# Kernel optimization log

Measured on AMD Instinct MI355X. Metric: run time of the kernel, lower is better.

Reference implementation:

```python
import jax, jax.numpy as jnp
import numpy as np

D_MODEL = 768
N_HEADS = 12
NUM_EXPERTS = 4
TOP_K = 2
SPAN_LEN = 64
GATE_HIDDEN = 128


def setup_inputs() -> dict:
    key = jax.random.key(0)
    ks = jax.random.split(key, 14)
    B, T, C, E = 4, 4096, D_MODEL, NUM_EXPERTS
    s = 0.02
    return {
        "hidden_states": jax.random.normal(ks[0], (B, T, C), jnp.float32),
        "Wq": jax.random.normal(ks[1], (E, C, C), jnp.float32) * s,
        "bq": jnp.zeros((E, C), jnp.float32),
        "Wk": jax.random.normal(ks[2], (E, C, C), jnp.float32) * s,
        "bk": jnp.zeros((E, C), jnp.float32),
        "Wv": jax.random.normal(ks[3], (E, C, C), jnp.float32) * s,
        "bv": jnp.zeros((E, C), jnp.float32),
        "gW1": jax.random.normal(ks[4], (GATE_HIDDEN, C), jnp.float32) * s,
        "gb1": jnp.zeros((GATE_HIDDEN,), jnp.float32),
        "gW2": jax.random.normal(ks[5], (E, GATE_HIDDEN), jnp.float32) * s,
        "gb2": jnp.zeros((E,), jnp.float32),
        "Wo": jax.random.normal(ks[6], (C, C), jnp.float32) * s,
        "bo": jnp.zeros((C,), jnp.float32),
    }


def _moe_proj(w, x, W, b):
    # per-expert projection then gate-weighted sum over experts
    # x: (B,N,S,C), W: (E,O,C), w: (B,N,E)
    proj = jnp.einsum("bnsc,eoc->ebnso", x, W)          # (E,B,N,S,C)
    out = jnp.einsum("bne,ebnso->bnso", w, proj)
    out = out + jnp.einsum("bne,eo->bno", w, b)[:, :, None, :]
    return out


def reference(hidden_states, Wq, bq, Wk, bk, Wv, bv, gW1, gb1, gW2, gb2, Wo, bo):
    B, T, C = hidden_states.shape
    S, H, E, K = SPAN_LEN, N_HEADS, NUM_EXPERTS, TOP_K
    Dh = C // H
    N = T // S  # T is a multiple of span_len -> no padding, all-ones masks
    x = hidden_states.reshape(B, N, S, C)

    # gating: mean-pool per span -> MLP -> top-k softmax scattered to E slots
    pooled = x.mean(axis=2)                                  # (B,N,C)
    h = jax.nn.relu(pooled @ gW1.T + gb1)
    logits = h @ gW2.T + gb2                                 # (B,N,E)
    vals, idx = jax.lax.top_k(logits, K)
    sm = jax.nn.softmax(vals, axis=-1)                       # (B,N,K)
    w = jnp.sum(jax.nn.one_hot(idx, E, dtype=sm.dtype) * sm[..., None], axis=-2)  # (B,N,E)
    entropy = -jnp.mean(jnp.sum(w * jnp.log(jnp.clip(w, 1e-9)), axis=-1))

    # gate-weighted expert QKV projections
    q = _moe_proj(w, x, Wq, bq).reshape(B, N, S, H, Dh)
    k = _moe_proj(w, x, Wk, bk).reshape(B, N, S, H, Dh)
    v = _moe_proj(w, x, Wv, bv).reshape(B, N, S, H, Dh)

    # per-span attention (mask is all ones; dropout in eval mode)
    scores = jnp.einsum("bnshd,bnthd->bnhst", q, k) / jnp.sqrt(jnp.float32(Dh))
    attn = jax.nn.softmax(scores, axis=-1)
    out = jnp.einsum("bnhst,bnthd->bnshd", attn, v).reshape(B, T, C)
    out = out @ Wo.T + bo
    return out, entropy
```

## Files before the change

### kernel.cpp

```cpp
#include <hip/hip_runtime.h>
#include <hip/hip_bf16.h>
#include <hip/hip_fp16.h>

typedef _Float16 f16;
typedef _Float16 f16x8 __attribute__((ext_vector_type(8)));
typedef _Float16 f16x4 __attribute__((ext_vector_type(4)));
typedef float f32x4 __attribute__((ext_vector_type(4)));

constexpr int B = 4;
constexpr int T = 4096;
constexpr int C = 768;
constexpr int NH = 12;
constexpr int DH = 64;
constexpr int E = 4;
constexpr int SPAN = 64;
constexpr int N = T / SPAN;
constexpr int BN = B * N;
constexpr int GH = 128;
constexpr int BTC = B * T * C;

constexpr int U_WE = E * C * C / 8;
constexpr int U_WO = C * C / 8;
constexpr int U_WTOT = 3 * U_WE + U_WO;

#define LGKM_BARRIER()                                      \
    do {                                                    \
        asm volatile("s_waitcnt lgkmcnt(0)" ::: "memory");  \
        __builtin_amdgcn_s_barrier();                       \
        __builtin_amdgcn_sched_barrier(0);                  \
    } while (0)

__global__ __launch_bounds__(768) void cvt_x_pool(
    const float* __restrict__ x, f16* __restrict__ x16,
    float* __restrict__ pooled) {
    int span = blockIdx.x;
    int tid = threadIdx.x;
    int u = tid % 96, rg = tid / 96;
    __shared__ float part[8][C];

    const float* xb = x + (size_t)span * SPAN * C;
    f16x8* xo = (f16x8*)x16 + (size_t)span * 6144;
    int kt = u >> 2, lg = u & 3;
    float a8[8] = {};
    #pragma unroll
    for (int j = 0; j < 8; ++j) {
        int r = rg * 8 + j;
        const float4* s = (const float4*)(xb + (size_t)r * C + u * 8);
        float4 A = s[0], Bv = s[1];
        f16x8 o;
        o[0] = (f16)A.x;  o[1] = (f16)A.y;  o[2] = (f16)A.z;  o[3] = (f16)A.w;
        o[4] = (f16)Bv.x; o[5] = (f16)Bv.y; o[6] = (f16)Bv.z; o[7] = (f16)Bv.w;
        int m = r >> 4, lr = r & 15;
        xo[(kt * 4 + m) * 64 + lg * 16 + lr] = o;
        a8[0] += A.x;  a8[1] += A.y;  a8[2] += A.z;  a8[3] += A.w;
        a8[4] += Bv.x; a8[5] += Bv.y; a8[6] += Bv.z; a8[7] += Bv.w;
    }
    #pragma unroll
    for (int j = 0; j < 8; ++j) part[rg][u * 8 + j] = a8[j];
    __syncthreads();
    float s = 0.f;
    #pragma unroll
    for (int g = 0; g < 8; ++g) s += part[g][tid];
    pooled[(size_t)span * C + tid] = s * (1.f / 64.f);
}

__global__ void cvt_w(const float* __restrict__ Wq, const float* __restrict__ Wk,
                      const float* __restrict__ Wv, const float* __restrict__ Wo,
                      f16* __restrict__ Wq16, f16* __restrict__ Wk16,
                      f16* __restrict__ Wv16, f16* __restrict__ Wo16) {
    int i = blockIdx.x * blockDim.x + threadIdx.x;
    int stride = gridDim.x * blockDim.x;
    for (; i < U_WTOT; i += stride) {
        const float* src; f16* dst; int u;
        bool frag = true;
        if (i < U_WE)               { src = Wq; dst = Wq16; u = i; }
        else if (i < 2 * U_WE)      { src = Wk; dst = Wk16; u = i - U_WE; }
        else if (i < 3 * U_WE)      { src = Wv; dst = Wv16; u = i - 2 * U_WE; }
        else                        { src = Wo; dst = Wo16; u = i - 3 * U_WE; frag = false; }
        float4 a = ((const float4*)src)[2 * u];
        float4 b = ((const float4*)src)[2 * u + 1];
        f16x8 o;
        o[0] = (f16)a.x; o[1] = (f16)a.y; o[2] = (f16)a.z; o[3] = (f16)a.w;
        o[4] = (f16)b.x; o[5] = (f16)b.y; o[6] = (f16)b.z; o[7] = (f16)b.w;
        if (frag) {
            int e   = u / (C * C / 8);
            int rem = u - e * (C * C / 8);
            int orow = rem / 96;
            int ku   = rem - orow * 96;
            int cb = orow >> 6, nn = (orow >> 4) & 3, lr = orow & 15;
            int kt = ku >> 2, lg = ku & 3;
            ((f16x8*)dst)[(size_t)(e * 12 + cb) * 6144 + (kt * 4 + nn) * 64 + lg * 16 + lr] = o;
        } else {
            ((f16x8*)dst)[u] = o;
        }
    }
}

__global__ __launch_bounds__(128) void gate_mlp(
    const float* __restrict__ pooled,
    const float* __restrict__ gW1, const float* __restrict__ gb1,
    const float* __restrict__ gW2, const float* __restrict__ gb2,
    int* __restrict__ eidx, float* __restrict__ ewts,
    float* __restrict__ ent_partial) {
    int span = blockIdx.x;
    int tid = threadIdx.x;
    __shared__ float pl[C];
    __shared__ float h[GH];
    __shared__ float logits[E];

    for (int c = tid; c < C; c += 128) pl[c] = pooled[(size_t)span * C + c];
    __syncthreads();

    {
        float acc = gb1[tid];
        const float* wrow = gW1 + (size_t)tid * C;
        #pragma unroll 8
        for (int c = 0; c < C; ++c) acc += pl[c] * wrow[c];
        h[tid] = acc > 0.f ? acc : 0.f;
    }
    __syncthreads();

    if (tid < E) {
        float acc = gb2[tid];
        const float* wrow = gW2 + (size_t)tid * GH;
        #pragma unroll 8
        for (int j = 0; j < GH; ++j) acc += h[j] * wrow[j];
        logits[tid] = acc;
    }
    __syncthreads();

    if (tid == 0) {
        int i0 = 0; float v0 = logits[0];
        for (int e = 1; e < E; ++e) { if (logits[e] > v0) { v0 = logits[e]; i0 = e; } }
        int i1 = -1; float v1 = -3.0e38f;
        for (int e = 0; e < E; ++e) { if (e != i0 && logits[e] > v1) { v1 = logits[e]; i1 = e; } }
        float bq_ = expf(v1 - v0);
        float s = 1.f + bq_;
        float sm0 = 1.f / s;
        float sm1 = bq_ / s;
        eidx[span * 2 + 0] = i0;
        eidx[span * 2 + 1] = i1;
        ewts[span * 2 + 0] = sm0;
        ewts[span * 2 + 1] = sm1;
        float p0 = fmaxf(sm0, 1e-9f), p1 = fmaxf(sm1, 1e-9f);
        ent_partial[span] = sm0 * logf(p0) + sm1 * logf(p1);
    }
}

__global__ void entropy_kernel(const float* __restrict__ ent_partial, float* __restrict__ out_ent) {
    __shared__ float sh[256];
    int tid = threadIdx.x;
    sh[tid] = ent_partial[tid];
    __syncthreads();
    for (int s = 128; s > 0; s >>= 1) {
        if (tid < s) sh[tid] += sh[tid + s];
        __syncthreads();
    }
    if (tid == 0) *out_ent = -sh[0] * (1.0f / (float)BN);
}

__global__ __launch_bounds__(256, 3) void qkv_mfma(
    const f16* __restrict__ xh,
    const f16* __restrict__ Wq16, const float* __restrict__ bq,
    const f16* __restrict__ Wk16, const float* __restrict__ bk,
    const f16* __restrict__ Wv16, const float* __restrict__ bv,
    const int* __restrict__ eidx, const float* __restrict__ ewts,
    f16* __restrict__ q16, f16* __restrict__ k16, f16* __restrict__ vt)
{
    int span  = blockIdx.x;
    int otile = blockIdx.y;
    int proj  = blockIdx.z;

    const f16* W; const float* bias; f16* out;
    if (proj == 0)      { W = Wq16; bias = bq; out = q16; }
    else if (proj == 1) { W = Wk16; bias = bk; out = k16; }
    else                { W = Wv16; bias = bv; out = vt; }

    int e0 = eidx[span * 2 + 0], e1 = eidx[span * 2 + 1];
    float w0 = ewts[span * 2 + 0], w1 = ewts[span * 2 + 1];
    f16 w0h = (f16)w0, w1h = (f16)w1;

    int tid = threadIdx.x;
    int lane = tid & 63, wv = tid >> 6;
    int lr = lane & 15, lg = lane >> 4;
    int cb = otile * 4 + wv;

    const f16x8* xu  = (const f16x8*)xh + (size_t)span * 6144 + lane;
    const f16x8* wu0 = (const f16x8*)W + ((size_t)e0 * 12 + cb) * 6144 + lane;
    const f16x8* wu1 = (const f16x8*)W + ((size_t)e1 * 12 + cb) * 6144 + lane;

    f32x4 acc[4][4] = {};

    #pragma unroll 4
    for (int kt = 0; kt < 24; ++kt) {
        f16x8 af[4], bf[4];
        #pragma unroll
        for (int m = 0; m < 4; ++m) af[m] = xu[(kt * 4 + m) * 64];
        #pragma unroll
        for (int n = 0; n < 4; ++n) {
            f16x8 b0 = wu0[(kt * 4 + n) * 64];
            f16x8 b1 = wu1[(kt * 4 + n) * 64];
            bf[n] = b0 * w0h + b1 * w1h;
        }
        #pragma unroll
        for (int m = 0; m < 4; ++m)
            #pragma unroll
            for (int n = 0; n < 4; ++n)
                acc[m][n] = __builtin_amdgcn_mfma_f32_16x16x32_f16(af[m], bf[n], acc[m][n], 0, 0, 0);
    }

    if (proj == 2) {
        f16* vtb = out + (size_t)span * C * 64;
        #pragma unroll
        for (int n = 0; n < 4; ++n) {
            int col = cb * 64 + n * 16 + lr;
            float be = w0 * bias[(size_t)e0 * C + col] + w1 * bias[(size_t)e1 * C + col];
            #pragma unroll
            for (int m = 0; m < 4; ++m) {
                f16x4 pk;
                #pragma unroll
                for (int r = 0; r < 4; ++r) pk[r] = (f16)(acc[m][n][r] + be);
                *(f16x4*)&vtb[(size_t)col * 64 + m * 16 + lg * 4] = pk;
            }
        }
    } else {
        f16* outb = out + (size_t)span * 64 * C;
        #pragma unroll
        for (int n = 0; n < 4; ++n) {
            int col = cb * 64 + n * 16 + lr;
            float be = w0 * bias[(size_t)e0 * C + col] + w1 * bias[(size_t)e1 * C + col];
            #pragma unroll
            for (int m = 0; m < 4; ++m) {
                #pragma unroll
                for (int r = 0; r < 4; ++r) {
                    int row = m * 16 + lg * 4 + r;
                    outb[(size_t)row * C + col] = (f16)(acc[m][n][r] + be);
                }
            }
        }
    }
}

__global__ __launch_bounds__(256) void attn_mfma(
    const f16* __restrict__ q16, const f16* __restrict__ k16,
    const f16* __restrict__ vt, f16* __restrict__ a16)
{
    int h = blockIdx.x, span = blockIdx.y;
    __shared__ __align__(16) f16 Klds[64 * 72];
    __shared__ __align__(16) f16 Vlds[64 * 72];
    __shared__ __align__(16) f16 Plds[64 * 72];

    int tid = threadIdx.x;
    int lane = tid & 63, mt = tid >> 6;
    int lr = lane & 15, lg = lane >> 4;

    const f16x8* ku = (const f16x8*)k16;
    const f16x8* vu = (const f16x8*)vt;
    #pragma unroll
    for (int i = 0; i < 2; ++i) {
        int id = tid + i * 256;
        int r = id >> 3, u = id & 7;
        *(f16x8*)&Klds[r * 72 + u * 8] = ku[(size_t)span * 6144 + (size_t)r * 96 + h * 8 + u];
        *(f16x8*)&Vlds[r * 72 + u * 8] = vu[(size_t)span * 6144 + (size_t)(h * 64 + r) * 8 + u];
    }
    const f16x8* qu = (const f16x8*)q16;
    f16x8 qa[2];
    #pragma unroll
    for (int kk = 0; kk < 2; ++kk)
        qa[kk] = qu[(size_t)span * 6144 + (size_t)(mt * 16 + lr) * 96 + h * 8 + kk * 4 + lg];

    LGKM_BARRIER();

    f32x4 accs[4] = {};
    #pragma unroll
    for (int nt = 0; nt < 4; ++nt) {
        #pragma unroll
        for (int kk = 0; kk < 2; ++kk) {
            f16x8 kb = *(const f16x8*)&Klds[(nt * 16 + lr) * 72 + kk * 32 + lg * 8];
            accs[nt] = __builtin_amdgcn_mfma_f32_16x16x32_f16(qa[kk], kb, accs[nt], 0, 0, 0);
        }
    }

    #pragma unroll
    for (int nt = 0; nt < 4; ++nt) accs[nt] *= 0.125f;
    f32x4 m4;
    #pragma unroll
    for (int r = 0; r < 4; ++r)
        m4[r] = fmaxf(fmaxf(accs[0][r], accs[1][r]), fmaxf(accs[2][r], accs[3][r]));
    #pragma unroll
    for (int st = 1; st < 16; st <<= 1) {
        #pragma unroll
        for (int r = 0; r < 4; ++r) m4[r] = fmaxf(m4[r], __shfl_xor(m4[r], st));
    }
    f32x4 ps[4];
    f32x4 sum4 = {0.f, 0.f, 0.f, 0.f};
    #pragma unroll
    for (int nt = 0; nt < 4; ++nt)
        #pragma unroll
        for (int r = 0; r < 4; ++r) {
            ps[nt][r] = __expf(accs[nt][r] - m4[r]);
            sum4[r] += ps[nt][r];
        }
    #pragma unroll
    for (int st = 1; st < 16; st <<= 1) {
        #pragma unroll
        for (int r = 0; r < 4; ++r) sum4[r] += __shfl_xor(sum4[r], st);
    }
    f32x4 inv4;
    #pragma unroll
    for (int r = 0; r < 4; ++r) inv4[r] = 1.0f / sum4[r];

    #pragma unroll
    for (int nt = 0; nt < 4; ++nt)
        #pragma unroll
        for (int r = 0; r < 4; ++r)
            Plds[(mt * 16 + lg * 4 + r) * 72 + nt * 16 + lr] = (f16)ps[nt][r];

    LGKM_BARRIER();

    f16x8 pa[2];
    #pragma unroll
    for (int kkt = 0; kkt < 2; ++kkt)
        pa[kkt] = *(const f16x8*)&Plds[(mt * 16 + lr) * 72 + kkt * 32 + lg * 8];
    f32x4 acco[4] = {};
    #pragma unroll
    for (int nt = 0; nt < 4; ++nt) {
        #pragma unroll
        for (int kkt = 0; kkt < 2; ++kkt) {
            f16x8 vb = *(const f16x8*)&Vlds[(nt * 16 + lr) * 72 + kkt * 32 + lg * 8];
            acco[nt] = __builtin_amdgcn_mfma_f32_16x16x32_f16(pa[kkt], vb, acco[nt], 0, 0, 0);
        }
    }

    #pragma unroll
    for (int nt = 0; nt < 4; ++nt)
        #pragma unroll
        for (int r = 0; r < 4; ++r)
            Klds[(mt * 16 + lg * 4 + r) * 72 + nt * 16 + lr] = (f16)(acco[nt][r] * inv4[r]);

    LGKM_BARRIER();

    int row = mt * 16 + (lane >> 2);
    int u2 = (lane & 3) * 2;
    f16x8 o0 = *(const f16x8*)&Klds[row * 72 + u2 * 8];
    f16x8 o1 = *(const f16x8*)&Klds[row * 72 + u2 * 8 + 8];
    f16x8* au = (f16x8*)a16;
    au[(size_t)span * 6144 + (size_t)row * 96 + h * 8 + u2]     = o0;
    au[(size_t)span * 6144 + (size_t)row * 96 + h * 8 + u2 + 1] = o1;
}

__global__ __launch_bounds__(512) void outproj_mfma(
    const f16* __restrict__ ah, const f16* __restrict__ Wo16,
    const float* __restrict__ bo, float* __restrict__ Y)
{
    int rt = blockIdx.x;
    int otile = blockIdx.y;

    __shared__ f16x8 as_u[128 * 8];
    __shared__ f16x8 ws_u[256 * 8];

    const f16x8* au  = (const f16x8*)(ah + (size_t)rt * 128 * C);
    const f16x8* Wou = (const f16x8*)(Wo16 + (size_t)otile * 256 * C);

    int tid = threadIdx.x;
    int lane = tid & 63, wv = tid >> 6;
    int lr = lane & 15, lg = lane >> 4;
    int wm = (wv >> 2) * 64;
    int wn = (wv & 3) * 64;

    f32x4 acc[4][4] = {};

    f16x8 ar_[2], wr_[4];
    #pragma unroll
    for (int i = 0; i < 2; ++i) {
        int id = tid + i * 512;
        ar_[i] = au[(size_t)(id >> 3) * 96 + (id & 7)];
    }
    #pragma unroll
    for (int i = 0; i < 4; ++i) {
        int id = tid + i * 512;
        wr_[i] = Wou[(size_t)(id >> 3) * 96 + (id & 7)];
    }

    for (int kc8 = 0; kc8 < 96; kc8 += 8) {
        #pragma unroll
        for (int i = 0; i < 2; ++i) {
            int id = tid + i * 512;
            int r = id >> 3, u = id & 7;
            as_u[r * 8 + (u ^ (r & 7))] = ar_[i];
        }
        #pragma unroll
        for (int i = 0; i < 4; ++i) {
            int id = tid + i * 512;
            int r = id >> 3, u = id & 7;
            ws_u[r * 8 + (u ^ (r & 7))] = wr_[i];
        }

        if (kc8 < 88) {
            int kn = kc8 + 8;
            #pragma unroll
            for (int i = 0; i < 2; ++i) {
                int id = tid + i * 512;
                ar_[i] = au[(size_t)(id >> 3) * 96 + kn + (id & 7)];
            }
            #pragma unroll
            for (int i = 0; i < 4; ++i) {
                int id = tid + i * 512;
                wr_[i] = Wou[(size_t)(id >> 3) * 96 + kn + (id & 7)];
            }
        }

        LGKM_BARRIER();

        #pragma unroll
        for (int kk = 0; kk < 2; ++kk) {
            int ub = kk * 4 + lg;
            f16x8 afrag[4], bfrag[4];
            #pragma unroll
            for (int m = 0; m < 4; ++m) {
                int r = wm + m * 16 + lr;
                afrag[m] = as_u[r * 8 + (ub ^ (r & 7))];
            }
            #pragma unroll
            for (int n = 0; n < 4; ++n) {
                int r = wn + n * 16 + lr;
                bfrag[n] = ws_u[r * 8 + (ub ^ (r & 7))];
            }
            #pragma unroll
            for (int m = 0; m < 4; ++m)
                #pragma unroll
                for (int n = 0; n < 4; ++n)
                    acc[m][n] = __builtin_amdgcn_mfma_f32_16x16x32_f16(afrag[m], bfrag[n], acc[m][n], 0, 0, 0);
        }

        LGKM_BARRIER();
    }

    #pragma unroll
    for (int n = 0; n < 4; ++n) {
        int col = otile * 256 + wn + n * 16 + lr;
        float be = bo[col];
        #pragma unroll
        for (int m = 0; m < 4; ++m) {
            #pragma unroll
            for (int r = 0; r < 4; ++r) {
                int row = rt * 128 + wm + m * 16 + lg * 4 + r;
                Y[(size_t)row * C + col] = acc[m][n][r] + be;
            }
        }
    }
}

extern "C" void kernel_launch(void* const* d_in, const int* in_sizes, int n_in,
                              void* d_out, int out_size, void* d_ws, size_t ws_size,
                              hipStream_t stream) {
    const float* x   = (const float*)d_in[0];
    const float* Wq  = (const float*)d_in[1];
    const float* bq  = (const float*)d_in[2];
    const float* Wk  = (const float*)d_in[3];
    const float* bk  = (const float*)d_in[4];
    const float* Wv  = (const float*)d_in[5];
    const float* bv  = (const float*)d_in[6];
    const float* gW1 = (const float*)d_in[7];
    const float* gb1 = (const float*)d_in[8];
    const float* gW2 = (const float*)d_in[9];
    const float* gb2 = (const float*)d_in[10];
    const float* Wo  = (const float*)d_in[11];
    const float* bo  = (const float*)d_in[12];

    float* out = (float*)d_out;

    char* ws = (char*)d_ws;
    const size_t h_btc = (size_t)BTC * sizeof(f16);
    f16* x16  = (f16*)(ws);
    f16* q16  = (f16*)(ws + 1 * h_btc);
    f16* k16  = (f16*)(ws + 2 * h_btc);
    f16* vt16 = (f16*)(ws + 3 * h_btc);
    f16* a16  = (f16*)(ws + 4 * h_btc);
    size_t off = 5 * h_btc;
    const size_t wsz = (size_t)E * C * C * sizeof(f16);
    f16* Wq16 = (f16*)(ws + off); off += wsz;
    f16* Wk16 = (f16*)(ws + off); off += wsz;
    f16* Wv16 = (f16*)(ws + off); off += wsz;
    f16* Wo16 = (f16*)(ws + off); off += (size_t)C * C * sizeof(f16);
    int*   eidx = (int*)(ws + off); off += 2048;
    float* ewts = (float*)(ws + off); off += 2048;
    float* entp = (float*)(ws + off); off += 1024;
    float* pooled = (float*)(ws + off); off += (size_t)BN * C * sizeof(float);

    cvt_x_pool<<<dim3(BN), dim3(768), 0, stream>>>(x, x16, pooled);
    cvt_w<<<dim3(1024), dim3(256), 0, stream>>>(Wq, Wk, Wv, Wo,
                                                Wq16, Wk16, Wv16, Wo16);
    gate_mlp<<<dim3(BN), dim3(128), 0, stream>>>(pooled, gW1, gb1, gW2, gb2,
                                                 eidx, ewts, entp);
    entropy_kernel<<<dim3(1), dim3(256), 0, stream>>>(entp, out + BTC);

    qkv_mfma<<<dim3(BN, 3, 3), dim3(256), 0, stream>>>(x16, Wq16, bq, Wk16, bk, Wv16, bv,
                                                       eidx, ewts, q16, k16, vt16);
    attn_mfma<<<dim3(NH, BN), dim3(256), 0, stream>>>(q16, k16, vt16, a16);
    outproj_mfma<<<dim3(128, 3), dim3(512), 0, stream>>>(a16, Wo16, bo, out);
}
```

Baseline: 239.4 us.

## Stage fp16 conversions through swizzled LDS and software-pipeline QKV weight loads

The x and Wq/Wk/Wv fp16 conversions now go through an XOR-swizzled shared-memory tile, so the fragment-layout global writes become contiguous instead of scattered. Wo gets its own simple conversion kernel. The QKV MFMA loop is restructured to double-buffer expert weight fragments a k-step ahead and raises wave priority around the MFMA bursts, so load latency overlaps with compute. This adds LDS use (about 96KB per block in the conversion kernels) and register pressure in the QKV kernel.

```diff
diff --git a/kernel.cpp b/kernel.cpp
--- a/kernel.cpp
+++ b/kernel.cpp
@@ -19,9 +19,7 @@
 constexpr int GH = 128;
 constexpr int BTC = B * T * C;
 
-constexpr int U_WE = E * C * C / 8;
 constexpr int U_WO = C * C / 8;
-constexpr int U_WTOT = 3 * U_WE + U_WO;
 
 #define LGKM_BARRIER()                                      \
     do {                                                    \
@@ -36,11 +34,10 @@
     int span = blockIdx.x;
     int tid = threadIdx.x;
     int u = tid % 96, rg = tid / 96;
+    __shared__ f16x8 xlds[6144];
     __shared__ float part[8][C];
 
     const float* xb = x + (size_t)span * SPAN * C;
-    f16x8* xo = (f16x8*)x16 + (size_t)span * 6144;
-    int kt = u >> 2, lg = u & 3;
     float a8[8] = {};
     #pragma unroll
     for (int j = 0; j < 8; ++j) {
@@ -50,8 +47,7 @@
         f16x8 o;
         o[0] = (f16)A.x;  o[1] = (f16)A.y;  o[2] = (f16)A.z;  o[3] = (f16)A.w;
         o[4] = (f16)Bv.x; o[5] = (f16)Bv.y; o[6] = (f16)Bv.z; o[7] = (f16)Bv.w;
-        int m = r >> 4, lr = r & 15;
-        xo[(kt * 4 + m) * 64 + lg * 16 + lr] = o;
+        xlds[r * 96 + (u & ~7) + ((u & 7) ^ (r & 7))] = o;
         a8[0] += A.x;  a8[1] += A.y;  a8[2] += A.z;  a8[3] += A.w;
         a8[4] += Bv.x; a8[5] += Bv.y; a8[6] += Bv.z; a8[7] += Bv.w;
     }
@@ -62,37 +58,66 @@
     #pragma unroll
     for (int g = 0; g < 8; ++g) s += part[g][tid];
     pooled[(size_t)span * C + tid] = s * (1.f / 64.f);
-}
-
-__global__ void cvt_w(const float* __restrict__ Wq, const float* __restrict__ Wk,
-                      const float* __restrict__ Wv, const float* __restrict__ Wo,
-                      f16* __restrict__ Wq16, f16* __restrict__ Wk16,
-                      f16* __restrict__ Wv16, f16* __restrict__ Wo16) {
+
+    f16x8* xo = (f16x8*)x16 + (size_t)span * 6144;
+    #pragma unroll
+    for (int j = 0; j < 8; ++j) {
+        int un = tid + j * 768;
+        int lr = un & 15, lg = (un >> 4) & 3, m = (un >> 6) & 3, kt = un >> 8;
+        int row = m * 16 + lr, ku = kt * 4 + lg;
+        xo[un] = xlds[row * 96 + (ku & ~7) + ((ku & 7) ^ (row & 7))];
+    }
+}
+
+__global__ __launch_bounds__(768) void cvt_w_frag(
+    const float* __restrict__ Wq, const float* __restrict__ Wk,
+    const float* __restrict__ Wv,
+    f16* __restrict__ Wq16, f16* __restrict__ Wk16, f16* __restrict__ Wv16) {
+    int slice = blockIdx.x;
+    int tsel  = blockIdx.y;
+    const float* src; f16* dst;
+    if (tsel == 0)      { src = Wq; dst = Wq16; }
+    else if (tsel == 1) { src = Wk; dst = Wk16; }
+    else                { src = Wv; dst = Wv16; }
+    int e = slice / 12, cb = slice % 12;
+
+    __shared__ f16x8 wlds[6144];
+    int tid = threadIdx.x;
+
+    const float* wb = src + ((size_t)e * C + cb * 64) * C;
+    #pragma unroll
+    for (int j = 0; j < 8; ++j) {
+        int g = tid + j * 768;
+        int row = g / 96, ku = g % 96;
+        const float4* sp = (const float4*)(wb + (size_t)row * C + ku * 8);
+        float4 A = sp[0], Bv = sp[1];
+        f16x8 o;
+        o[0] = (f16)A.x;  o[1] = (f16)A.y;  o[2] = (f16)A.z;  o[3] = (f16)A.w;
+        o[4] = (f16)Bv.x; o[5] = (f16)Bv.y; o[6] = (f16)Bv.z; o[7] = (f16)Bv.w;
+        wlds[row * 96 + (ku & ~7) + ((ku & 7) ^ (row & 7))] = o;
+    }
+    __syncthreads();
+
+    f16x8* wo = (f16x8*)dst + (size_t)slice * 6144;
+    #pragma unroll
+    for (int j = 0; j < 8; ++j) {
+        int un = tid + j * 768;
+        int lr = un & 15, lg = (un >> 4) & 3, nn = (un >> 6) & 3, kt = un >> 8;
+        int row = nn * 16 + lr, ku = kt * 4 + lg;
+        wo[un] = wlds[row * 96 + (ku & ~7) + ((ku & 7) ^ (row & 7))];
+    }
+}
+
+__global__ void cvt_wo(const float* __restrict__ Wo, f16* __restrict__ Wo16) {
     int i = blockIdx.x * blockDim.x + threadIdx.x;
     int stride = gridDim.x * blockDim.x;
-    for (; i < U_WTOT; i += stride) {
-        const float* src; f16* dst; int u;
-        bool frag = true;
-        if (i < U_WE)               { src = Wq; dst = Wq16; u = i; }
-        else if (i < 2 * U_WE)      { src = Wk; dst = Wk16; u = i - U_WE; }
-        else if (i < 3 * U_WE)      { src = Wv; dst = Wv16; u = i - 2 * U_WE; }
-        else                        { src = Wo; dst = Wo16; u = i - 3 * U_WE; frag = false; }
-        float4 a = ((const float4*)src)[2 * u];
-        float4 b = ((const float4*)src)[2 * u + 1];
+    for (; i < U_WO; i += stride) {
+        float4 a = ((const float4*)Wo)[2 * i];
+        float4 b = ((const float4*)Wo)[2 * i + 1];
         f16x8 o;
         o[0] = (f16)a.x; o[1] = (f16)a.y; o[2] = (f16)a.z; o[3] = (f16)a.w;
         o[4] = (f16)b.x; o[5] = (f16)b.y; o[6] = (f16)b.z; o[7] = (f16)b.w;
-        if (frag) {
-            int e   = u / (C * C / 8);
-            int rem = u - e * (C * C / 8);
-            int orow = rem / 96;
-            int ku   = rem - orow * 96;
-            int cb = orow >> 6, nn = (orow >> 4) & 3, lr = orow & 15;
-            int kt = ku >> 2, lg = ku & 3;
-            ((f16x8*)dst)[(size_t)(e * 12 + cb) * 6144 + (kt * 4 + nn) * 64 + lg * 16 + lr] = o;
-        } else {
-            ((f16x8*)dst)[u] = o;
-        }
+        ((f16x8*)Wo16)[i] = o;
     }
 }
 
@@ -191,22 +216,56 @@
 
     f32x4 acc[4][4] = {};
 
-    #pragma unroll 4
-    for (int kt = 0; kt < 24; ++kt) {
-        f16x8 af[4], bf[4];
-        #pragma unroll
-        for (int m = 0; m < 4; ++m) af[m] = xu[(kt * 4 + m) * 64];
+    f16x8 b0A[4], b1A[4], b0B[4], b1B[4];
+    #pragma unroll
+    for (int n = 0; n < 4; ++n) { b0A[n] = wu0[n * 64]; b1A[n] = wu1[n * 64]; }
+
+    for (int kt2 = 0; kt2 < 12; ++kt2) {
+        int ktA = kt2 * 2, ktB = ktA + 1;
+
         #pragma unroll
         for (int n = 0; n < 4; ++n) {
-            f16x8 b0 = wu0[(kt * 4 + n) * 64];
-            f16x8 b1 = wu1[(kt * 4 + n) * 64];
-            bf[n] = b0 * w0h + b1 * w1h;
-        }
-        #pragma unroll
-        for (int m = 0; m < 4; ++m)
-            #pragma unroll
-            for (int n = 0; n < 4; ++n)
-                acc[m][n] = __builtin_amdgcn_mfma_f32_16x16x32_f16(af[m], bf[n], acc[m][n], 0, 0, 0);
+            b0B[n] = wu0[(ktB * 4 + n) * 64];
+            b1B[n] = wu1[(ktB * 4 + n) * 64];
+        }
+
+        {
+            f16x8 af[4];
+            #pragma unroll
+            for (int m = 0; m < 4; ++m) af[m] = xu[(ktA * 4 + m) * 64];
+            __builtin_amdgcn_s_setprio(1);
+            #pragma unroll
+            for (int n = 0; n < 4; ++n) {
+                f16x8 bf = b0A[n] * w0h + b1A[n] * w1h;
+                #pragma unroll
+                for (int m = 0; m < 4; ++m)
+                    acc[m][n] = __builtin_amdgcn_mfma_f32_16x16x32_f16(af[m], bf, acc[m][n], 0, 0, 0);
+            }
+            __builtin_amdgcn_s_setprio(0);
+        }
+
+        if (kt2 < 11) {
+            #pragma unroll
+            for (int n = 0; n < 4; ++n) {
+                b0A[n] = wu0[((ktA + 2) * 4 + n) * 64];
+                b1A[n] = wu1[((ktA + 2) * 4 + n) * 64];
+            }
+        }
+
+        {
+            f16x8 af[4];
+            #pragma unroll
+            for (int m = 0; m < 4; ++m) af[m] = xu[(ktB * 4 + m) * 64];
+            __builtin_amdgcn_s_setprio(1);
+            #pragma unroll
+            for (int n = 0; n < 4; ++n) {
+                f16x8 bf = b0B[n] * w0h + b1B[n] * w1h;
+                #pragma unroll
+                for (int m = 0; m < 4; ++m)
+                    acc[m][n] = __builtin_amdgcn_mfma_f32_16x16x32_f16(af[m], bf, acc[m][n], 0, 0, 0);
+            }
+            __builtin_amdgcn_s_setprio(0);
+        }
     }
 
     if (proj == 2) {
@@ -489,8 +548,9 @@
     float* pooled = (float*)(ws + off); off += (size_t)BN * C * sizeof(float);
 
     cvt_x_pool<<<dim3(BN), dim3(768), 0, stream>>>(x, x16, pooled);
-    cvt_w<<<dim3(1024), dim3(256), 0, stream>>>(Wq, Wk, Wv, Wo,
-                                                Wq16, Wk16, Wv16, Wo16);
+    cvt_w_frag<<<dim3(48, 3), dim3(768), 0, stream>>>(Wq, Wk, Wv,
+                                                      Wq16, Wk16, Wv16);
+    cvt_wo<<<dim3(288), dim3(256), 0, stream>>>(Wo, Wo16);
     gate_mlp<<<dim3(BN), dim3(128), 0, stream>>>(pooled, gW1, gb1, gW2, gb2,
                                                  eidx, ewts, entp);
     entropy_kernel<<<dim3(1), dim3(256), 0, stream>>>(entp, out + BTC);
```

Result: faster. 209.8 us (-12.4%).
